# Performance work log

Measured on AMD Instinct MI355X. Metric: run time of the kernel, lower is better.

## Reference

```python
import jax, jax.numpy as jnp
import numpy as np

B, S, D = 8, 1024, 1024
H = 16
D_HEAD = D // H
RANK = 256
NC = 64
NE = 64
KC = 16  # top_k_compress
KE = 8   # top_k_expand


def setup_inputs() -> dict:
    key = jax.random.key(0)
    ks = jax.random.split(key, 9)
    rn = lambda k, sh, s=1.0: jax.random.normal(k, sh, jnp.float32) * s
    return {
        "x": rn(ks[0], (B, S, D)),
        "importance": jax.random.uniform(ks[1], (B, S), jnp.float32),
        "W_compress": rn(ks[2], (NC, D), 1.0 / np.sqrt(D)),
        "W_Q": rn(ks[3], (NE, D), 1.0 / np.sqrt(D)),
        "W_K": rn(ks[4], (NE, D), 1.0 / np.sqrt(D)),
        "W_V": rn(ks[5], (NE, D), 1.0 / np.sqrt(D)),
        "compress_neurons": rn(ks[6], (NC, D, RANK), 1.0 / np.sqrt(D)),
        "expand_pool": rn(ks[7], (NE, RANK, D), 1.0 / np.sqrt(RANK)),
        "W_O": rn(ks[8], (D, D), 1.0 / np.sqrt(D)),
    }


def _route(x, importance, W, k):
    """Per-token softmax router, importance-aggregated, top-k renormalized."""
    pref = jax.nn.softmax(jnp.einsum('bsd,nd->bsn', x, W), axis=-1)  # [B,S,n]
    w = jnp.einsum('bs,bsn->bn', importance, pref)                   # [B,n]
    w = w / (w.sum(-1, keepdims=True) + 1e-8)
    tw, ti = jax.lax.top_k(w, k)                                     # [B,k]
    tw = tw / (tw.sum(-1, keepdims=True) + 1e-8)
    return tw, ti


def reference(x, importance, W_compress, W_Q, W_K, W_V, compress_neurons, expand_pool, W_O):
    # --- GlobalRouters.get_attention_weights ---
    cw, ci = _route(x, importance, W_compress, KC)
    qw, qi = _route(x, importance, W_Q, KE)
    kw, ki = _route(x, importance, W_K, KE)
    vw, vi = _route(x, importance, W_V, KE)

    # --- NeuronCircuit.forward ---
    # gather + mix compress neurons: [B,KC,D,R] -> [B,D,R]
    shared_c = jnp.einsum('bk,bkdr->bdr', cw, compress_neurons[ci])
    h = jnp.einsum('bsd,bdr->bsr', x, shared_c)  # [B,S,R]

    eQ = jnp.einsum('bk,bkrd->brd', qw, expand_pool[qi])
    eK = jnp.einsum('bk,bkrd->brd', kw, expand_pool[ki])
    eV = jnp.einsum('bk,bkrd->brd', vw, expand_pool[vi])

    def heads(t):  # [B,S,D] -> [B,H,S,d_head]
        return t.reshape(B, S, H, D_HEAD).transpose(0, 2, 1, 3)

    Q = heads(jnp.einsum('bsr,brd->bsd', h, eQ))
    K = heads(jnp.einsum('bsr,brd->bsd', h, eK))
    V = heads(jnp.einsum('bsr,brd->bsd', h, eV))

    scale = 1.0 / np.sqrt(D_HEAD)
    scores = jnp.einsum('bhqd,bhkd->bhqk', Q, K) * scale
    causal = jnp.tril(jnp.ones((S, S), dtype=bool))
    scores = jnp.where(causal, scores, jnp.finfo(scores.dtype).min)
    attn = jax.nn.softmax(scores, axis=-1)
    out = jnp.einsum('bhqk,bhkd->bhqd', attn, V)
    out = out.transpose(0, 2, 1, 3).reshape(B, S, D)
    return jnp.einsum('bsd,ed->bse', out, W_O)  # expand_O (Linear, no bias)
```

## Files before the change

### kernel.cpp

```cpp
#include <hip/hip_runtime.h>

typedef __attribute__((ext_vector_type(8))) short short8;
typedef __attribute__((ext_vector_type(4))) short short4v;
typedef __attribute__((ext_vector_type(4))) float f32x4;
typedef unsigned short u16;
typedef unsigned int u32;

__device__ __forceinline__ float bf2f(u16 h) {
    return __uint_as_float(((u32)h) << 16);
}
__device__ __forceinline__ u16 f2bf(float f) {
    u32 u = __float_as_uint(f);
    u32 r = u + 0x7fffu + ((u >> 16) & 1u);
    return (u16)(r >> 16);
}
__device__ __forceinline__ u32 pack_bf(float a, float b) {
    return __builtin_amdgcn_perm(__float_as_uint(b), __float_as_uint(a), 0x07060302u);
}

__device__ __forceinline__ void async_copy16(const void* g, void* l) {
    __builtin_amdgcn_global_load_lds(
        (const __attribute__((address_space(1))) void*)g,
        (__attribute__((address_space(3))) void*)l, 16, 0, 0);
}

__global__ __launch_bounds__(256) void cvt_split(
    const float* __restrict__ in, u16* __restrict__ hi, u16* __restrict__ lo, int n4)
{
    int i = blockIdx.x * 256 + threadIdx.x;
    if (i >= n4) return;
    float4 v = ((const float4*)in)[i];
    short4v h, l;
    float vv[4] = {v.x, v.y, v.z, v.w};
#pragma unroll
    for (int j = 0; j < 4; j++) {
        u16 hb = f2bf(vv[j]);
        h[j] = (short)hb;
        l[j] = (short)f2bf(vv[j] - bf2f(hb));
    }
    ((short4v*)hi)[i] = h;
    ((short4v*)lo)[i] = l;
}

__global__ __launch_bounds__(256) void cvt_split_w4(
    const float* __restrict__ w0, const float* __restrict__ w1,
    const float* __restrict__ w2, const float* __restrict__ w3,
    u16* __restrict__ hi, u16* __restrict__ lo)
{
    const int r = blockIdx.x >> 6;
    const float* src = (r == 0) ? w0 : (r == 1) ? w1 : (r == 2) ? w2 : w3;
    int i = (blockIdx.x & 63) * 256 + threadIdx.x;
    float4 v = ((const float4*)src)[i];
    short4v h, l;
    float vv[4] = {v.x, v.y, v.z, v.w};
#pragma unroll
    for (int j = 0; j < 4; j++) {
        u16 hb = f2bf(vv[j]);
        h[j] = (short)hb;
        l[j] = (short)f2bf(vv[j] - bf2f(hb));
    }
    ((short4v*)(hi + (long)r * 65536))[i] = h;
    ((short4v*)(lo + (long)r * 65536))[i] = l;
}

__global__ __launch_bounds__(256) void cvt_bf(
    const float* __restrict__ in, u16* __restrict__ out, int n4)
{
    int i = blockIdx.x * 256 + threadIdx.x;
    if (i >= n4) return;
    float4 v = ((const float4*)in)[i];
    short4v h;
    h[0] = (short)f2bf(v.x); h[1] = (short)f2bf(v.y);
    h[2] = (short)f2bf(v.z); h[3] = (short)f2bf(v.w);
    ((short4v*)out)[i] = h;
}

template <typename CT, int BK>
__global__ __launch_bounds__(256) void gemm_bt(
    const u16* __restrict__ A, long lda, long bsA,
    const u16* __restrict__ Bm, long ldb, long bsB,
    CT* __restrict__ C, long ldc, long bsC, int K, float cscale)
{
    constexpr int NC = BK / 32;
    constexpr int RB = 16 * BK;
    __shared__ __align__(16) u16 lsA[128 * BK];
    __shared__ __align__(16) u16 lsB[128 * BK];
    const int tid = threadIdx.x;
    const int wave = tid >> 6, lane = tid & 63;
    const int quad = lane >> 4, l15 = lane & 15;
    const int wm = wave >> 1, wn = wave & 1;
    const long m0 = (long)blockIdx.x * 128, n0 = (long)blockIdx.y * 128;
    A  += (long)blockIdx.z * bsA;
    Bm += (long)blockIdx.z * bsB;
    C  += (long)blockIdx.z * bsC;
    const int srow = lane >> 2, scol = (lane & 3) * 8;

    f32x4 acc[4][4];
#pragma unroll
    for (int i = 0; i < 4; i++)
#pragma unroll
        for (int j = 0; j < 4; j++) acc[i][j] = (f32x4){0.f, 0.f, 0.f, 0.f};

    const u16* ga0 = A + (m0 + (wave * 2 + 0) * 16 + srow) * lda + scol;
    const u16* ga1 = A + (m0 + (wave * 2 + 1) * 16 + srow) * lda + scol;
    const u16* gb0 = Bm + (n0 + (wave * 2 + 0) * 16 + srow) * ldb + scol;
    const u16* gb1 = Bm + (n0 + (wave * 2 + 1) * 16 + srow) * ldb + scol;
    u16* laA = &lsA[(wave * 2 + 0) * RB];
    u16* laB = &lsA[(wave * 2 + 1) * RB];
    u16* lbA = &lsB[(wave * 2 + 0) * RB];
    u16* lbB = &lsB[(wave * 2 + 1) * RB];

    for (int kk = 0; kk < K; kk += BK) {
#pragma unroll
        for (int c = 0; c < NC; c++) {
            async_copy16(ga0 + kk + c * 32, laA + c * 512);
            async_copy16(ga1 + kk + c * 32, laB + c * 512);
            async_copy16(gb0 + kk + c * 32, lbA + c * 512);
            async_copy16(gb1 + kk + c * 32, lbB + c * 512);
        }
        __syncthreads();
#pragma unroll
        for (int kb = 0; kb < NC; kb++) {
            short8 af[4], bf[4];
#pragma unroll
            for (int mt = 0; mt < 4; mt++)
                af[mt] = *(const short8*)&lsA[(wm * 4 + mt) * RB + kb * 512 + l15 * 32 + quad * 8];
#pragma unroll
            for (int nt = 0; nt < 4; nt++)
                bf[nt] = *(const short8*)&lsB[(wn * 4 + nt) * RB + kb * 512 + l15 * 32 + quad * 8];
#pragma unroll
            for (int mt = 0; mt < 4; mt++)
#pragma unroll
                for (int nt = 0; nt < 4; nt++)
                    acc[mt][nt] = __builtin_amdgcn_mfma_f32_16x16x32_bf16(
                        af[mt], bf[nt], acc[mt][nt], 0, 0, 0);
        }
        __syncthreads();
    }
#pragma unroll
    for (int mt = 0; mt < 4; mt++) {
        const long rowb = m0 + wm * 64 + mt * 16 + quad * 4;
#pragma unroll
        for (int nt = 0; nt < 4; nt++) {
            const long col = n0 + wn * 64 + nt * 16 + l15;
#pragma unroll
            for (int r = 0; r < 4; r++) {
                const float v = acc[mt][nt][r] * cscale;
                if constexpr (sizeof(CT) == 2)
                    C[(rowb + r) * ldc + col] = f2bf(v);
                else
                    C[(rowb + r) * ldc + col] = v;
            }
        }
    }
}

__global__ __launch_bounds__(256) void gemm_qkv(
    const u16* __restrict__ hbuf, const u16* __restrict__ eQT,
    const u16* __restrict__ eKT, const u16* __restrict__ eVT,
    u16* __restrict__ Qb, u16* __restrict__ Kb, u16* __restrict__ VTb)
{
    __shared__ __align__(16) u16 lsA[128 * 64];
    __shared__ __align__(16) u16 lsB[128 * 64];
    const int z = blockIdx.z;
    const int sel = z >> 3, bbz = z & 7;
    const long ab = (long)bbz * 262144;
    const u16* A  = ((sel == 2) ? eVT : hbuf) + ab;
    const u16* Bm = ((sel == 0) ? eQT : (sel == 1) ? eKT : hbuf) + ab;
    u16* C = ((sel == 0) ? Qb : (sel == 1) ? Kb : VTb) + (long)bbz * 1048576;
    const float cscale = (sel == 0) ? 0.180336880111f : 1.0f;

    const int tid = threadIdx.x;
    const int wave = tid >> 6, lane = tid & 63;
    const int quad = lane >> 4, l15 = lane & 15;
    const int wm = wave >> 1, wn = wave & 1;
    const long m0 = (long)blockIdx.x * 128, n0 = (long)blockIdx.y * 128;
    const int srow = lane >> 2, scol = (lane & 3) * 8;

    f32x4 acc[4][4];
#pragma unroll
    for (int i = 0; i < 4; i++)
#pragma unroll
        for (int j = 0; j < 4; j++) acc[i][j] = (f32x4){0.f, 0.f, 0.f, 0.f};

    const u16* ga0 = A + (m0 + (wave * 2 + 0) * 16 + srow) * 256 + scol;
    const u16* ga1 = A + (m0 + (wave * 2 + 1) * 16 + srow) * 256 + scol;
    const u16* gb0 = Bm + (n0 + (wave * 2 + 0) * 16 + srow) * 256 + scol;
    const u16* gb1 = Bm + (n0 + (wave * 2 + 1) * 16 + srow) * 256 + scol;
    u16* laA = &lsA[(wave * 2 + 0) * 1024];
    u16* laB = &lsA[(wave * 2 + 1) * 1024];
    u16* lbA = &lsB[(wave * 2 + 0) * 1024];
    u16* lbB = &lsB[(wave * 2 + 1) * 1024];

    for (int kk = 0; kk < 256; kk += 64) {
        async_copy16(ga0 + kk,      laA);
        async_copy16(ga0 + kk + 32, laA + 512);
        async_copy16(ga1 + kk,      laB);
        async_copy16(ga1 + kk + 32, laB + 512);
        async_copy16(gb0 + kk,      lbA);
        async_copy16(gb0 + kk + 32, lbA + 512);
        async_copy16(gb1 + kk,      lbB);
        async_copy16(gb1 + kk + 32, lbB + 512);
        __syncthreads();
#pragma unroll
        for (int kb = 0; kb < 2; kb++) {
            short8 af[4], bf[4];
#pragma unroll
            for (int mt = 0; mt < 4; mt++)
                af[mt] = *(const short8*)&lsA[(wm * 4 + mt) * 1024 + kb * 512 + l15 * 32 + quad * 8];
#pragma unroll
            for (int nt = 0; nt < 4; nt++)
                bf[nt] = *(const short8*)&lsB[(wn * 4 + nt) * 1024 + kb * 512 + l15 * 32 + quad * 8];
#pragma unroll
            for (int mt = 0; mt < 4; mt++)
#pragma unroll
                for (int nt = 0; nt < 4; nt++)
                    acc[mt][nt] = __builtin_amdgcn_mfma_f32_16x16x32_bf16(
                        af[mt], bf[nt], acc[mt][nt], 0, 0, 0);
        }
        __syncthreads();
    }
#pragma unroll
    for (int mt = 0; mt < 4; mt++) {
        const long rowb = m0 + wm * 64 + mt * 16 + quad * 4;
#pragma unroll
        for (int nt = 0; nt < 4; nt++) {
            const long col = n0 + wn * 64 + nt * 16 + l15;
#pragma unroll
            for (int r = 0; r < 4; r++)
                C[(rowb + r) * 1024 + col] = f2bf(acc[mt][nt][r] * cscale);
        }
    }
}

__global__ __launch_bounds__(256) void gemm_router(
    const u16* __restrict__ Ah, const u16* __restrict__ Al,
    const u16* __restrict__ Bh, const u16* __restrict__ Bl,
    float* __restrict__ C0, float* __restrict__ C1, float* __restrict__ C2)
{
    __shared__ __align__(16) u16 lsA[128 * 128];
    __shared__ __align__(16) u16 lsB[128 * 128];
    const int seg = blockIdx.z;
    const u16* A = (seg == 1) ? Al : Ah;
    const u16* B = (seg == 2) ? Bl : Bh;
    float* C = (seg == 0) ? C0 : (seg == 1) ? C1 : C2;
    const int tid = threadIdx.x;
    const int wave = tid >> 6, lane = tid & 63;
    const int quad = lane >> 4, l15 = lane & 15;
    const int wm = wave >> 1, wn = wave & 1;
    const long m0 = (long)blockIdx.x * 128, n0 = (long)blockIdx.y * 128;
    const int srow = lane >> 2, scol = (lane & 3) * 8;
    const u16* ga = A + (m0 + (wave * 2) * 16 + srow) * 1024 + scol;
    const u16* gb = B + (n0 + (wave * 2) * 16 + srow) * 1024 + scol;
    u16* laA = &lsA[(wave * 2 + 0) * 2048];
    u16* laB = &lsA[(wave * 2 + 1) * 2048];
    u16* lbA = &lsB[(wave * 2 + 0) * 2048];
    u16* lbB = &lsB[(wave * 2 + 1) * 2048];

    f32x4 acc[4][4];
#pragma unroll
    for (int i = 0; i < 4; i++)
#pragma unroll
        for (int j = 0; j < 4; j++) acc[i][j] = (f32x4){0.f, 0.f, 0.f, 0.f};

    for (int kk = 0; kk < 1024; kk += 128) {
#pragma unroll
        for (int c = 0; c < 4; c++) {
            async_copy16(ga + kk + c * 32,         laA + c * 512);
            async_copy16(ga + 16384 + kk + c * 32, laB + c * 512);
            async_copy16(gb + kk + c * 32,         lbA + c * 512);
            async_copy16(gb + 16384 + kk + c * 32, lbB + c * 512);
        }
        __syncthreads();
#pragma unroll
        for (int kb = 0; kb < 4; kb++) {
            short8 af[4], bf[4];
#pragma unroll
            for (int mt = 0; mt < 4; mt++)
                af[mt] = *(const short8*)&lsA[(wm * 4 + mt) * 2048 + kb * 512 + l15 * 32 + quad * 8];
#pragma unroll
            for (int nt = 0; nt < 4; nt++)
                bf[nt] = *(const short8*)&lsB[(wn * 4 + nt) * 2048 + kb * 512 + l15 * 32 + quad * 8];
#pragma unroll
            for (int mt = 0; mt < 4; mt++)
#pragma unroll
                for (int nt = 0; nt < 4; nt++)
                    acc[mt][nt] = __builtin_amdgcn_mfma_f32_16x16x32_bf16(
                        af[mt], bf[nt], acc[mt][nt], 0, 0, 0);
        }
        __syncthreads();
    }
#pragma unroll
    for (int mt = 0; mt < 4; mt++) {
        const long rowb = m0 + wm * 64 + mt * 16 + quad * 4;
#pragma unroll
        for (int nt = 0; nt < 4; nt++) {
            const long col = n0 + wn * 64 + nt * 16 + l15;
#pragma unroll
            for (int r = 0; r < 4; r++)
                C[(rowb + r) * 256 + col] = acc[mt][nt][r];
        }
    }
}

__global__ __launch_bounds__(128) void router_agg(
    const float* __restrict__ l0, const float* __restrict__ l1,
    const float* __restrict__ l2, const float* __restrict__ imp,
    float* __restrict__ w_raw)
{
    __shared__ float pref[32][257];
    const int tid = threadIdx.x;
    const int tl = tid >> 2, r = tid & 3;
    const int s = blockIdx.x * 32 + tl;
    const int b = s >> 10;
    const long off = (long)s * 256 + r * 64;
    float v[64];
#pragma unroll
    for (int i = 0; i < 16; i++) {
        float4 f0 = ((const float4*)(l0 + off))[i];
        float4 f1 = ((const float4*)(l1 + off))[i];
        float4 f2 = ((const float4*)(l2 + off))[i];
        v[i * 4 + 0] = f0.x + f1.x + f2.x;
        v[i * 4 + 1] = f0.y + f1.y + f2.y;
        v[i * 4 + 2] = f0.z + f1.z + f2.z;
        v[i * 4 + 3] = f0.w + f1.w + f2.w;
    }
    float mx = v[0];
#pragma unroll
    for (int i = 1; i < 64; i++) mx = fmaxf(mx, v[i]);
    float sum = 0.f;
#pragma unroll
    for (int i = 0; i < 64; i++) { v[i] = __expf(v[i] - mx); sum += v[i]; }
    const float scale = imp[s] / sum;
#pragma unroll
    for (int i = 0; i < 64; i++) pref[tl][r * 64 + i] = v[i] * scale;
    __syncthreads();
#pragma unroll
    for (int half = 0; half < 2; half++) {
        const int idx = tid + half * 128;
        const int r2 = idx >> 6, n = idx & 63;
        float acc = 0.f;
#pragma unroll 8
        for (int t = 0; t < 32; t++) acc += pref[t][r2 * 64 + n];
        atomicAdd(&w_raw[(r2 * 8 + b) * 64 + n], acc);
    }
}

__global__ void topk_kernel(const float* __restrict__ w_raw,
                            float* __restrict__ topw, int* __restrict__ topi)
{
    const int r = blockIdx.x >> 3, b = blockIdx.x & 7;
    const int lane = threadIdx.x;
    const int k = (r == 0) ? 16 : 8;
    float w = w_raw[(r * 8 + b) * 64 + lane];
    float tot = w;
    for (int o2 = 32; o2 >= 1; o2 >>= 1) tot += __shfl_xor(tot, o2);
    w = w / (tot + 1e-8f);
    __shared__ float tw[16];
    __shared__ int ti[16];
    float cur = w;
    float ssum = 0.f;
    for (int j = 0; j < k; j++) {
        float m = cur; int mi = lane;
        for (int o2 = 32; o2 >= 1; o2 >>= 1) {
            float om = __shfl_xor(m, o2); int oi = __shfl_xor(mi, o2);
            if (om > m || (om == m && oi < mi)) { m = om; mi = oi; }
        }
        if (lane == 0) { tw[j] = m; ti[j] = mi; }
        ssum += m;
        if (lane == mi) cur = -1e30f;
    }
    __syncthreads();
    if (lane < 16) {
        topw[(r * 8 + b) * 16 + lane] = (lane < k) ? tw[lane] / (ssum + 1e-8f) : 0.f;
        topi[(r * 8 + b) * 16 + lane] = (lane < k) ? ti[lane] : 0;
    }
}

__global__ __launch_bounds__(256) void gather_mix(
    const float* __restrict__ pool, const float* __restrict__ topw,
    const int* __restrict__ topi, u16* __restrict__ out,
    int I, int J, int k)
{
    __shared__ float tile[64][65];
    const int b = blockIdx.z;
    const long IJ = (long)I * J;
    const int i0 = blockIdx.x * 64, j0 = blockIdx.y * 64;
    const float* tw = topw + b * 16;
    const int* ti = topi + b * 16;
    const int tid = threadIdx.x;
    const int il = tid >> 2, jg = tid & 3;
    float acc[16];
#pragma unroll
    for (int m = 0; m < 16; m++) acc[m] = 0.f;
    for (int kk = 0; kk < k; kk++) {
        const float wgt = tw[kk];
        const long n = ti[kk];
        const float* src = pool + n * IJ + (long)(i0 + il) * J + j0 + jg * 16;
        float4 a0 = ((const float4*)src)[0];
        float4 a1 = ((const float4*)src)[1];
        float4 a2 = ((const float4*)src)[2];
        float4 a3 = ((const float4*)src)[3];
        acc[0] += wgt * a0.x;  acc[1] += wgt * a0.y;
        acc[2] += wgt * a0.z;  acc[3] += wgt * a0.w;
        acc[4] += wgt * a1.x;  acc[5] += wgt * a1.y;
        acc[6] += wgt * a1.z;  acc[7] += wgt * a1.w;
        acc[8] += wgt * a2.x;  acc[9] += wgt * a2.y;
        acc[10] += wgt * a2.z; acc[11] += wgt * a2.w;
        acc[12] += wgt * a3.x; acc[13] += wgt * a3.y;
        acc[14] += wgt * a3.z; acc[15] += wgt * a3.w;
    }
#pragma unroll
    for (int m = 0; m < 16; m++) tile[il][jg * 16 + m] = acc[m];
    __syncthreads();
    const int jl = tid >> 2, ig = tid & 3;
    short8 o0, o1;
#pragma unroll
    for (int m = 0; m < 8; m++) {
        o0[m] = (short)f2bf(tile[ig * 16 + m][jl]);
        o1[m] = (short)f2bf(tile[ig * 16 + 8 + m][jl]);
    }
    u16* dst = out + (long)b * IJ + (long)(j0 + jl) * I + i0 + ig * 16;
    *(short8*)dst = o0;
    *(short8*)(dst + 8) = o1;
}

__global__ __launch_bounds__(256) void gather_mix3(
    const float* __restrict__ pool, const float* __restrict__ topw,
    const int* __restrict__ topi, u16* __restrict__ eQT,
    u16* __restrict__ eKT, u16* __restrict__ eVT)
{
    __shared__ float tile[64][65];
    const int z = blockIdx.z;
    const int r = z >> 3, b = z & 7;
    u16* out = (r == 0) ? eQT : (r == 1) ? eKT : eVT;
    const long IJ = 262144;
    const int i0 = blockIdx.x * 64, j0 = blockIdx.y * 64;
    const float* tw = topw + (1 + r) * 128 + b * 16;
    const int* ti = topi + (1 + r) * 128 + b * 16;
    const int tid = threadIdx.x;
    const int il = tid >> 2, jg = tid & 3;
    float acc[16];
#pragma unroll
    for (int m = 0; m < 16; m++) acc[m] = 0.f;
    for (int kk = 0; kk < 8; kk++) {
        const float wgt = tw[kk];
        const long n = ti[kk];
        const float* src = pool + n * IJ + (long)(i0 + il) * 1024 + j0 + jg * 16;
        float4 a0 = ((const float4*)src)[0];
        float4 a1 = ((const float4*)src)[1];
        float4 a2 = ((const float4*)src)[2];
        float4 a3 = ((const float4*)src)[3];
        acc[0] += wgt * a0.x;  acc[1] += wgt * a0.y;
        acc[2] += wgt * a0.z;  acc[3] += wgt * a0.w;
        acc[4] += wgt * a1.x;  acc[5] += wgt * a1.y;
        acc[6] += wgt * a1.z;  acc[7] += wgt * a1.w;
        acc[8] += wgt * a2.x;  acc[9] += wgt * a2.y;
        acc[10] += wgt * a2.z; acc[11] += wgt * a2.w;
        acc[12] += wgt * a3.x; acc[13] += wgt * a3.y;
        acc[14] += wgt * a3.z; acc[15] += wgt * a3.w;
    }
#pragma unroll
    for (int m = 0; m < 16; m++) tile[il][jg * 16 + m] = acc[m];
    __syncthreads();
    const int jl = tid >> 2, ig = tid & 3;
    short8 o0, o1;
#pragma unroll
    for (int m = 0; m < 8; m++) {
        o0[m] = (short)f2bf(tile[ig * 16 + m][jl]);
        o1[m] = (short)f2bf(tile[ig * 16 + 8 + m][jl]);
    }
    u16* dst = out + (long)b * IJ + (long)(j0 + jl) * 256 + i0 + ig * 16;
    *(short8*)dst = o0;
    *(short8*)(dst + 8) = o1;
}

__global__ __launch_bounds__(256, 2) void flash_attn(
    const u16* __restrict__ Qg, const u16* __restrict__ Kg,
    const u16* __restrict__ Vt, u16* __restrict__ Og)
{
    __shared__ __align__(16) u16 plds[4][32 * 72];
    const int tid = threadIdx.x;
    const int wv = tid >> 6, lane = tid & 63;
    const int quad = lane >> 4, l15 = lane & 15;
    const int p = blockIdx.x;
    const int bidx = (p & 7) * 64 + (p >> 3);
    const int gw = bidx * 4 + wv;
    const int pr = gw & 15;
    const int bh = gw >> 4;
    const int hh = bh & 15, bb = bh >> 4;
    const long SD = 1024L * 1024L;
    const u16* Qb = Qg + (long)bb * SD + hh * 64;
    const u16* Kb = Kg + (long)bb * SD + hh * 64;
    const u16* Vb = Vt + (long)bb * SD + (long)hh * 64 * 1024;
    u16* myp = plds[wv];

    for (int half = 0; half < 2; half++) {
        const int qt = half ? (31 - pr) : pr;
        const int q0 = qt * 32;

        short8 qf[2][2];
#pragma unroll
        for (int mt = 0; mt < 2; mt++)
#pragma unroll
            for (int kb = 0; kb < 2; kb++)
                qf[mt][kb] = *(const short8*)(Qb + (long)(q0 + mt * 16 + l15) * 1024 + kb * 32 + quad * 8);

        f32x4 o[2][4];
        float mrow[2] = {-3e38f, -3e38f}, lrow[2] = {0.f, 0.f};
#pragma unroll
        for (int mt = 0; mt < 2; mt++)
#pragma unroll
            for (int nt = 0; nt < 4; nt++) o[mt][nt] = (f32x4){0.f, 0.f, 0.f, 0.f};

        const int ntile = (q0 + 95) >> 6;
        short8 kf[4][2], kn[4][2];
#pragma unroll
        for (int kt = 0; kt < 4; kt++)
#pragma unroll
            for (int kb = 0; kb < 2; kb++)
                kf[kt][kb] = *(const short8*)(Kb + (long)(kt * 16 + l15) * 1024 + kb * 32 + quad * 8);

        for (int it = 0; it < ntile; it++) {
            const int k2 = it * 64;
            const bool last = (it == ntile - 1);
            f32x4 st[4][2];
            __builtin_amdgcn_s_setprio(1);
#pragma unroll
            for (int kt = 0; kt < 4; kt++)
#pragma unroll
                for (int q_ = 0; q_ < 2; q_++) {
                    f32x4 z = (f32x4){0.f, 0.f, 0.f, 0.f};
                    z = __builtin_amdgcn_mfma_f32_16x16x32_bf16(kf[kt][0], qf[q_][0], z, 0, 0, 0);
                    z = __builtin_amdgcn_mfma_f32_16x16x32_bf16(kf[kt][1], qf[q_][1], z, 0, 0, 0);
                    st[kt][q_] = z;
                }
            __builtin_amdgcn_s_setprio(0);
            short8 vf[4][2];
#pragma unroll
            for (int nt = 0; nt < 4; nt++)
#pragma unroll
                for (int kh = 0; kh < 2; kh++)
                    vf[nt][kh] = *(const short8*)(Vb + (long)(nt * 16 + l15) * 1024 + k2 + kh * 32 + quad * 8);
            if (it + 1 < ntile) {
#pragma unroll
                for (int kt = 0; kt < 4; kt++)
#pragma unroll
                    for (int kb = 0; kb < 2; kb++)
                        kn[kt][kb] = *(const short8*)(Kb + (long)(k2 + 64 + kt * 16 + l15) * 1024 + kb * 32 + quad * 8);
            }
            float cm2[2];
#pragma unroll
            for (int q_ = 0; q_ < 2; q_++) {
                if (last) {
#pragma unroll
                    for (int kt = 0; kt < 4; kt++)
#pragma unroll
                        for (int r = 0; r < 4; r++)
                            if (k2 + kt * 16 + quad * 4 + r > q0 + q_ * 16 + l15)
                                st[kt][q_][r] = -3e38f;
                }
                float t0 = fmaxf(fmaxf(st[0][q_][0], st[0][q_][1]), fmaxf(st[0][q_][2], st[0][q_][3]));
                float t1 = fmaxf(fmaxf(st[1][q_][0], st[1][q_][1]), fmaxf(st[1][q_][2], st[1][q_][3]));
                float t2 = fmaxf(fmaxf(st[2][q_][0], st[2][q_][1]), fmaxf(st[2][q_][2], st[2][q_][3]));
                float t3 = fmaxf(fmaxf(st[3][q_][0], st[3][q_][1]), fmaxf(st[3][q_][2], st[3][q_][3]));
                float cm = fmaxf(fmaxf(t0, t1), fmaxf(t2, t3));
                cm = fmaxf(cm, __shfl_xor(cm, 16));
                cm = fmaxf(cm, __shfl_xor(cm, 32));
                cm2[q_] = cm;
            }
            const float grow = fmaxf(cm2[0] - mrow[0], cm2[1] - mrow[1]);
            const bool resc = !__all(grow <= 8.0f);
            float am[2] = {1.f, 1.f};
            if (resc) {
#pragma unroll
                for (int q_ = 0; q_ < 2; q_++) {
                    const float mn = fmaxf(mrow[q_], cm2[q_]);
                    am[q_] = exp2f(mrow[q_] - mn);
                    mrow[q_] = mn;
                }
            }
#pragma unroll
            for (int q_ = 0; q_ < 2; q_++) {
                const float moff = 0.00281502f - mrow[q_];
                float s4[4];
#pragma unroll
                for (int kt = 0; kt < 4; kt++) {
                    float p0 = exp2f(st[kt][q_][0] + moff);
                    float p1 = exp2f(st[kt][q_][1] + moff);
                    float p2 = exp2f(st[kt][q_][2] + moff);
                    float p3 = exp2f(st[kt][q_][3] + moff);
                    s4[kt] = (p0 + p1) + (p2 + p3);
                    u32 w0 = pack_bf(p0, p1);
                    u32 w1 = pack_bf(p2, p3);
                    *(uint2*)&myp[(q_ * 16 + l15) * 72 + kt * 16 + quad * 4] = make_uint2(w0, w1);
                }
                float rs = (s4[0] + s4[1]) + (s4[2] + s4[3]);
                rs += __shfl_xor(rs, 16);
                rs += __shfl_xor(rs, 32);
                lrow[q_] = lrow[q_] * am[q_] + rs;
            }
            if (resc) {
                float av[2][4];
#pragma unroll
                for (int mt = 0; mt < 2; mt++)
#pragma unroll
                    for (int r = 0; r < 4; r++)
                        av[mt][r] = __shfl(am[mt], quad * 4 + r);
#pragma unroll
                for (int mt = 0; mt < 2; mt++)
#pragma unroll
                    for (int nt = 0; nt < 4; nt++)
#pragma unroll
                        for (int r = 0; r < 4; r++) o[mt][nt][r] *= av[mt][r];
            }
            asm volatile("s_waitcnt lgkmcnt(0)" ::: "memory");
            short8 pf0[2], pf1[2];
#pragma unroll
            for (int kh = 0; kh < 2; kh++) {
                pf0[kh] = *(const short8*)&myp[(l15) * 72 + kh * 32 + quad * 8];
                pf1[kh] = *(const short8*)&myp[(16 + l15) * 72 + kh * 32 + quad * 8];
            }
            __builtin_amdgcn_s_setprio(1);
#pragma unroll
            for (int nt = 0; nt < 4; nt++)
#pragma unroll
                for (int kh = 0; kh < 2; kh++) {
                    o[0][nt] = __builtin_amdgcn_mfma_f32_16x16x32_bf16(pf0[kh], vf[nt][kh], o[0][nt], 0, 0, 0);
                    o[1][nt] = __builtin_amdgcn_mfma_f32_16x16x32_bf16(pf1[kh], vf[nt][kh], o[1][nt], 0, 0, 0);
                }
            __builtin_amdgcn_s_setprio(0);
            if (it + 1 < ntile) {
#pragma unroll
                for (int kt = 0; kt < 4; kt++)
#pragma unroll
                    for (int kb = 0; kb < 2; kb++) kf[kt][kb] = kn[kt][kb];
            }
        }
#pragma unroll
        for (int mt = 0; mt < 2; mt++)
#pragma unroll
            for (int r = 0; r < 4; r++) {
                const float li = 1.0f / __shfl(lrow[mt], quad * 4 + r);
                const long row = q0 + mt * 16 + quad * 4 + r;
#pragma unroll
                for (int nt = 0; nt < 4; nt++)
                    Og[(long)bb * SD + row * 1024 + hh * 64 + nt * 16 + l15] =
                        f2bf(o[mt][nt][r] * li);
            }
    }
}

extern "C" void kernel_launch(void* const* d_in, const int* in_sizes, int n_in,
                              void* d_out, int out_size, void* d_ws, size_t ws_size,
                              hipStream_t stream)
{
    const float* x   = (const float*)d_in[0];
    const float* imp = (const float*)d_in[1];
    const float* cn  = (const float*)d_in[6];
    const float* ep  = (const float*)d_in[7];
    const float* Wo  = (const float*)d_in[8];
    float* outp = (float*)d_out;
    char* ws = (char*)d_ws;

    u16* xh = (u16*)d_out;
    u16* xl = xh + 8388608;

    u16*   Wh     = (u16*)(ws + 0);
    u16*   Wl     = (u16*)(ws + 524288);
    u16*   Wobf   = (u16*)(ws + 1048576);
    float* w_raw  = (float*)(ws + 3145728);
    float* topw   = (float*)(ws + 3153920);
    int*   topi   = (int*)(ws + 3155968);
    float* logit0 = (float*)(ws + 4194304);
    float* logit1 = (float*)(ws + 33554432);
    float* logit2 = (float*)(ws + 41943040);
    u16*   scT    = (u16*)(ws + 12582912);
    u16*   eQT    = (u16*)(ws + 16777216);
    u16*   Kb     = (u16*)(ws + 4194304);
    u16*   hbuf   = (u16*)(ws + 20971520);
    u16*   eKT    = (u16*)(ws + 25165824);
    u16*   eVT    = (u16*)(ws + 29360128);
    u16*   Qb     = (u16*)(ws + 33554432);
    u16*   VTb    = (u16*)(ws + 50331648);
    u16*   aout   = (u16*)(ws + 67108864);

    cvt_split<<<dim3(8192), 256, 0, stream>>>(x, xh, xl, 2097152);
    cvt_split_w4<<<dim3(256), 256, 0, stream>>>(
        (const float*)d_in[2], (const float*)d_in[3],
        (const float*)d_in[4], (const float*)d_in[5], Wh, Wl);
    cvt_bf<<<dim3(1024), 256, 0, stream>>>(Wo, Wobf, 262144);
    hipMemsetAsync(w_raw, 0, 4 * 8 * 64 * 4, stream);

    gemm_router<<<dim3(64, 2, 3), 256, 0, stream>>>(
        xh, xl, Wh, Wl, logit0, logit1, logit2);
    router_agg<<<dim3(256), 128, 0, stream>>>(logit0, logit1, logit2, imp, w_raw);
    topk_kernel<<<dim3(32), 64, 0, stream>>>(w_raw, topw, topi);
    gather_mix<<<dim3(16, 4, 8), 256, 0, stream>>>(cn, topw + 0 * 128, topi + 0 * 128, scT, 1024, 256, 16);
    gather_mix3<<<dim3(4, 16, 24), 256, 0, stream>>>(ep, topw, topi, eQT, eKT, eVT);
    gemm_bt<u16, 128><<<dim3(8, 2, 8), 256, 0, stream>>>(
        xh, 1024, 1048576, scT, 1024, 262144, hbuf, 256, 262144, 1024, 1.0f);
    gemm_qkv<<<dim3(8, 8, 24), 256, 0, stream>>>(hbuf, eQT, eKT, eVT, Qb, Kb, VTb);
    flash_attn<<<dim3(512), 256, 0, stream>>>(Qb, Kb, VTb, aout);
    gemm_bt<float, 128><<<dim3(64, 8, 1), 256, 0, stream>>>(
        aout, 1024, 0, Wobf, 1024, 0, outp, 1024, 0, 1024, 1.0f);
}
```

Before: 398.5 us.

## Split-K the router and h GEMMs to fill more CUs

The router GEMM grid is split along K into two halves, doubling blocks from 384 to 768, and router_agg now sums six partial logit buffers. The x·shared_c GEMM that used only 128 blocks is replaced by a 4-way split-K kernel (512 blocks) writing fp32 partials, followed by a reduction kernel that converts the sum to bf16. This targets under-occupancy of the GPU on these small-grid GEMMs, at the cost of extra fp32 partial traffic and one more kernel launch.

```diff
diff --git a/kernel.cpp b/kernel.cpp
--- a/kernel.cpp
+++ b/kernel.cpp
@@ -155,20 +155,17 @@
     }
 }
 
-__global__ __launch_bounds__(256) void gemm_qkv(
-    const u16* __restrict__ hbuf, const u16* __restrict__ eQT,
-    const u16* __restrict__ eKT, const u16* __restrict__ eVT,
-    u16* __restrict__ Qb, u16* __restrict__ Kb, u16* __restrict__ VTb)
+__global__ __launch_bounds__(256) void gemm_h4(
+    const u16* __restrict__ xh, const u16* __restrict__ scT,
+    float* __restrict__ P)
 {
     __shared__ __align__(16) u16 lsA[128 * 64];
     __shared__ __align__(16) u16 lsB[128 * 64];
     const int z = blockIdx.z;
-    const int sel = z >> 3, bbz = z & 7;
-    const long ab = (long)bbz * 262144;
-    const u16* A  = ((sel == 2) ? eVT : hbuf) + ab;
-    const u16* Bm = ((sel == 0) ? eQT : (sel == 1) ? eKT : hbuf) + ab;
-    u16* C = ((sel == 0) ? Qb : (sel == 1) ? Kb : VTb) + (long)bbz * 1048576;
-    const float cscale = (sel == 0) ? 0.180336880111f : 1.0f;
+    const int ks = z >> 3, bz = z & 7;
+    const u16* A  = xh  + (long)bz * 1048576 + ks * 256;
+    const u16* Bm = scT + (long)bz * 262144  + ks * 256;
+    float* C = P + (long)z * 262144;
 
     const int tid = threadIdx.x;
     const int wave = tid >> 6, lane = tid & 63;
@@ -183,10 +180,10 @@
 #pragma unroll
         for (int j = 0; j < 4; j++) acc[i][j] = (f32x4){0.f, 0.f, 0.f, 0.f};
 
-    const u16* ga0 = A + (m0 + (wave * 2 + 0) * 16 + srow) * 256 + scol;
-    const u16* ga1 = A + (m0 + (wave * 2 + 1) * 16 + srow) * 256 + scol;
-    const u16* gb0 = Bm + (n0 + (wave * 2 + 0) * 16 + srow) * 256 + scol;
-    const u16* gb1 = Bm + (n0 + (wave * 2 + 1) * 16 + srow) * 256 + scol;
+    const u16* ga0 = A + (m0 + (wave * 2 + 0) * 16 + srow) * 1024 + scol;
+    const u16* ga1 = A + (m0 + (wave * 2 + 1) * 16 + srow) * 1024 + scol;
+    const u16* gb0 = Bm + (n0 + (wave * 2 + 0) * 16 + srow) * 1024 + scol;
+    const u16* gb1 = Bm + (n0 + (wave * 2 + 1) * 16 + srow) * 1024 + scol;
     u16* laA = &lsA[(wave * 2 + 0) * 1024];
     u16* laB = &lsA[(wave * 2 + 1) * 1024];
     u16* lbA = &lsB[(wave * 2 + 0) * 1024];
@@ -228,30 +225,125 @@
             const long col = n0 + wn * 64 + nt * 16 + l15;
 #pragma unroll
             for (int r = 0; r < 4; r++)
-                C[(rowb + r) * 1024 + col] = f2bf(acc[mt][nt][r] * cscale);
-        }
-    }
-}
-
-__global__ __launch_bounds__(256) void gemm_router(
-    const u16* __restrict__ Ah, const u16* __restrict__ Al,
-    const u16* __restrict__ Bh, const u16* __restrict__ Bl,
-    float* __restrict__ C0, float* __restrict__ C1, float* __restrict__ C2)
-{
-    __shared__ __align__(16) u16 lsA[128 * 128];
-    __shared__ __align__(16) u16 lsB[128 * 128];
-    const int seg = blockIdx.z;
-    const u16* A = (seg == 1) ? Al : Ah;
-    const u16* B = (seg == 2) ? Bl : Bh;
-    float* C = (seg == 0) ? C0 : (seg == 1) ? C1 : C2;
+                C[(rowb + r) * 256 + col] = acc[mt][nt][r];
+        }
+    }
+}
+
+__global__ __launch_bounds__(256) void reduce_h4(
+    const float* __restrict__ P, u16* __restrict__ out)
+{
+    int i = blockIdx.x * 256 + threadIdx.x;
+    float4 a = ((const float4*)P)[i];
+    float4 b = ((const float4*)(P + 2097152))[i];
+    float4 c = ((const float4*)(P + 4194304))[i];
+    float4 d = ((const float4*)(P + 6291456))[i];
+    short4v h;
+    h[0] = (short)f2bf((a.x + b.x) + (c.x + d.x));
+    h[1] = (short)f2bf((a.y + b.y) + (c.y + d.y));
+    h[2] = (short)f2bf((a.z + b.z) + (c.z + d.z));
+    h[3] = (short)f2bf((a.w + b.w) + (c.w + d.w));
+    ((short4v*)out)[i] = h;
+}
+
+__global__ __launch_bounds__(256) void gemm_qkv(
+    const u16* __restrict__ hbuf, const u16* __restrict__ eQT,
+    const u16* __restrict__ eKT, const u16* __restrict__ eVT,
+    u16* __restrict__ Qb, u16* __restrict__ Kb, u16* __restrict__ VTb)
+{
+    __shared__ __align__(16) u16 lsA[128 * 64];
+    __shared__ __align__(16) u16 lsB[128 * 64];
+    const int z = blockIdx.z;
+    const int sel = z >> 3, bbz = z & 7;
+    const long ab = (long)bbz * 262144;
+    const u16* A  = ((sel == 2) ? eVT : hbuf) + ab;
+    const u16* Bm = ((sel == 0) ? eQT : (sel == 1) ? eKT : hbuf) + ab;
+    u16* C = ((sel == 0) ? Qb : (sel == 1) ? Kb : VTb) + (long)bbz * 1048576;
+    const float cscale = (sel == 0) ? 0.180336880111f : 1.0f;
+
     const int tid = threadIdx.x;
     const int wave = tid >> 6, lane = tid & 63;
     const int quad = lane >> 4, l15 = lane & 15;
     const int wm = wave >> 1, wn = wave & 1;
     const long m0 = (long)blockIdx.x * 128, n0 = (long)blockIdx.y * 128;
     const int srow = lane >> 2, scol = (lane & 3) * 8;
-    const u16* ga = A + (m0 + (wave * 2) * 16 + srow) * 1024 + scol;
-    const u16* gb = B + (n0 + (wave * 2) * 16 + srow) * 1024 + scol;
+
+    f32x4 acc[4][4];
+#pragma unroll
+    for (int i = 0; i < 4; i++)
+#pragma unroll
+        for (int j = 0; j < 4; j++) acc[i][j] = (f32x4){0.f, 0.f, 0.f, 0.f};
+
+    const u16* ga0 = A + (m0 + (wave * 2 + 0) * 16 + srow) * 256 + scol;
+    const u16* ga1 = A + (m0 + (wave * 2 + 1) * 16 + srow) * 256 + scol;
+    const u16* gb0 = Bm + (n0 + (wave * 2 + 0) * 16 + srow) * 256 + scol;
+    const u16* gb1 = Bm + (n0 + (wave * 2 + 1) * 16 + srow) * 256 + scol;
+    u16* laA = &lsA[(wave * 2 + 0) * 1024];
+    u16* laB = &lsA[(wave * 2 + 1) * 1024];
+    u16* lbA = &lsB[(wave * 2 + 0) * 1024];
+    u16* lbB = &lsB[(wave * 2 + 1) * 1024];
+
+    for (int kk = 0; kk < 256; kk += 64) {
+        async_copy16(ga0 + kk,      laA);
+        async_copy16(ga0 + kk + 32, laA + 512);
+        async_copy16(ga1 + kk,      laB);
+        async_copy16(ga1 + kk + 32, laB + 512);
+        async_copy16(gb0 + kk,      lbA);
+        async_copy16(gb0 + kk + 32, lbA + 512);
+        async_copy16(gb1 + kk,      lbB);
+        async_copy16(gb1 + kk + 32, lbB + 512);
+        __syncthreads();
+#pragma unroll
+        for (int kb = 0; kb < 2; kb++) {
+            short8 af[4], bf[4];
+#pragma unroll
+            for (int mt = 0; mt < 4; mt++)
+                af[mt] = *(const short8*)&lsA[(wm * 4 + mt) * 1024 + kb * 512 + l15 * 32 + quad * 8];
+#pragma unroll
+            for (int nt = 0; nt < 4; nt++)
+                bf[nt] = *(const short8*)&lsB[(wn * 4 + nt) * 1024 + kb * 512 + l15 * 32 + quad * 8];
+#pragma unroll
+            for (int mt = 0; mt < 4; mt++)
+#pragma unroll
+                for (int nt = 0; nt < 4; nt++)
+                    acc[mt][nt] = __builtin_amdgcn_mfma_f32_16x16x32_bf16(
+                        af[mt], bf[nt], acc[mt][nt], 0, 0, 0);
+        }
+        __syncthreads();
+    }
+#pragma unroll
+    for (int mt = 0; mt < 4; mt++) {
+        const long rowb = m0 + wm * 64 + mt * 16 + quad * 4;
+#pragma unroll
+        for (int nt = 0; nt < 4; nt++) {
+            const long col = n0 + wn * 64 + nt * 16 + l15;
+#pragma unroll
+            for (int r = 0; r < 4; r++)
+                C[(rowb + r) * 1024 + col] = f2bf(acc[mt][nt][r] * cscale);
+        }
+    }
+}
+
+__global__ __launch_bounds__(256) void gemm_router(
+    const u16* __restrict__ Ah, const u16* __restrict__ Al,
+    const u16* __restrict__ Bh, const u16* __restrict__ Bl,
+    float* __restrict__ Cbase)
+{
+    __shared__ __align__(16) u16 lsA[128 * 128];
+    __shared__ __align__(16) u16 lsB[128 * 128];
+    const int z = blockIdx.z;
+    const int seg = z >> 1, kh = z & 1;
+    const u16* A = (seg == 1) ? Al : Ah;
+    const u16* B = (seg == 2) ? Bl : Bh;
+    float* C = Cbase + (long)z * 2097152;
+    const int tid = threadIdx.x;
+    const int wave = tid >> 6, lane = tid & 63;
+    const int quad = lane >> 4, l15 = lane & 15;
+    const int wm = wave >> 1, wn = wave & 1;
+    const long m0 = (long)blockIdx.x * 128, n0 = (long)blockIdx.y * 128;
+    const int srow = lane >> 2, scol = (lane & 3) * 8;
+    const u16* ga = A + (m0 + (wave * 2) * 16 + srow) * 1024 + scol + kh * 512;
+    const u16* gb = B + (n0 + (wave * 2) * 16 + srow) * 1024 + scol + kh * 512;
     u16* laA = &lsA[(wave * 2 + 0) * 2048];
     u16* laB = &lsA[(wave * 2 + 1) * 2048];
     u16* lbA = &lsB[(wave * 2 + 0) * 2048];
@@ -263,7 +355,7 @@
 #pragma unroll
         for (int j = 0; j < 4; j++) acc[i][j] = (f32x4){0.f, 0.f, 0.f, 0.f};
 
-    for (int kk = 0; kk < 1024; kk += 128) {
+    for (int kk = 0; kk < 512; kk += 128) {
 #pragma unroll
         for (int c = 0; c < 4; c++) {
             async_copy16(ga + kk + c * 32,         laA + c * 512);
@@ -304,8 +396,7 @@
 }
 
 __global__ __launch_bounds__(128) void router_agg(
-    const float* __restrict__ l0, const float* __restrict__ l1,
-    const float* __restrict__ l2, const float* __restrict__ imp,
+    const float* __restrict__ lg, const float* __restrict__ imp,
     float* __restrict__ w_raw)
 {
     __shared__ float pref[32][257];
@@ -317,13 +408,16 @@
     float v[64];
 #pragma unroll
     for (int i = 0; i < 16; i++) {
-        float4 f0 = ((const float4*)(l0 + off))[i];
-        float4 f1 = ((const float4*)(l1 + off))[i];
-        float4 f2 = ((const float4*)(l2 + off))[i];
-        v[i * 4 + 0] = f0.x + f1.x + f2.x;
-        v[i * 4 + 1] = f0.y + f1.y + f2.y;
-        v[i * 4 + 2] = f0.z + f1.z + f2.z;
-        v[i * 4 + 3] = f0.w + f1.w + f2.w;
+        float4 f0 = ((const float4*)(lg + off))[i];
+        float4 f1 = ((const float4*)(lg + 2097152 + off))[i];
+        float4 f2 = ((const float4*)(lg + 2 * 2097152 + off))[i];
+        float4 f3 = ((const float4*)(lg + 3 * 2097152 + off))[i];
+        float4 f4 = ((const float4*)(lg + 4 * 2097152 + off))[i];
+        float4 f5 = ((const float4*)(lg + 5 * 2097152 + off))[i];
+        v[i * 4 + 0] = (f0.x + f1.x) + (f2.x + f3.x) + (f4.x + f5.x);
+        v[i * 4 + 1] = (f0.y + f1.y) + (f2.y + f3.y) + (f4.y + f5.y);
+        v[i * 4 + 2] = (f0.z + f1.z) + (f2.z + f3.z) + (f4.z + f5.z);
+        v[i * 4 + 3] = (f0.w + f1.w) + (f2.w + f3.w) + (f4.w + f5.w);
     }
     float mx = v[0];
 #pragma unroll
@@ -672,9 +766,8 @@
     float* w_raw  = (float*)(ws + 3145728);
     float* topw   = (float*)(ws + 3153920);
     int*   topi   = (int*)(ws + 3155968);
-    float* logit0 = (float*)(ws + 4194304);
-    float* logit1 = (float*)(ws + 33554432);
-    float* logit2 = (float*)(ws + 41943040);
+    float* logits = (float*)(ws + 33554432);
+    float* hpart  = (float*)(ws + 50331648);
     u16*   scT    = (u16*)(ws + 12582912);
     u16*   eQT    = (u16*)(ws + 16777216);
     u16*   Kb     = (u16*)(ws + 4194304);
@@ -692,14 +785,13 @@
     cvt_bf<<<dim3(1024), 256, 0, stream>>>(Wo, Wobf, 262144);
     hipMemsetAsync(w_raw, 0, 4 * 8 * 64 * 4, stream);
 
-    gemm_router<<<dim3(64, 2, 3), 256, 0, stream>>>(
-        xh, xl, Wh, Wl, logit0, logit1, logit2);
-    router_agg<<<dim3(256), 128, 0, stream>>>(logit0, logit1, logit2, imp, w_raw);
+    gemm_router<<<dim3(64, 2, 6), 256, 0, stream>>>(xh, xl, Wh, Wl, logits);
+    router_agg<<<dim3(256), 128, 0, stream>>>(logits, imp, w_raw);
     topk_kernel<<<dim3(32), 64, 0, stream>>>(w_raw, topw, topi);
     gather_mix<<<dim3(16, 4, 8), 256, 0, stream>>>(cn, topw + 0 * 128, topi + 0 * 128, scT, 1024, 256, 16);
     gather_mix3<<<dim3(4, 16, 24), 256, 0, stream>>>(ep, topw, topi, eQT, eKT, eVT);
-    gemm_bt<u16, 128><<<dim3(8, 2, 8), 256, 0, stream>>>(
-        xh, 1024, 1048576, scT, 1024, 262144, hbuf, 256, 262144, 1024, 1.0f);
+    gemm_h4<<<dim3(8, 2, 32), 256, 0, stream>>>(xh, scT, hpart);
+    reduce_h4<<<dim3(2048), 256, 0, stream>>>(hpart, hbuf);
     gemm_qkv<<<dim3(8, 8, 24), 256, 0, stream>>>(hbuf, eQT, eKT, eVT, Qb, Kb, VTb);
     flash_attn<<<dim3(512), 256, 0, stream>>>(Qb, Kb, VTb, aout);
     gemm_bt<float, 128><<<dim3(64, 8, 1), 256, 0, stream>>>(
```

Measured after the change: 409.2 us. +2.7%, slower.
